# Kernel optimization log

Hardware: AMD Instinct MI355X
Metric: run time of the kernel (lower is better)

The kernel has to match this reference:

```python
import jax, jax.numpy as jnp
import numpy as np

N = 100000
IN_CH = 128
HID = 16
HEADS = 8
OUT_CH = 16
E = 1600000
NEG_SLOPE = 0.2


def glorot(key, shape, fan_in, fan_out):
    lim = jnp.sqrt(6.0 / (fan_in + fan_out)).astype(jnp.float32)
    return jax.random.uniform(key, shape, jnp.float32, -lim, lim)


def setup_inputs() -> dict:
    key = jax.random.key(0)
    ks = jax.random.split(key, 10)
    x = jax.random.normal(ks[0], (N, IN_CH), jnp.float32)
    edge_index = jax.random.randint(ks[1], (2, E), 0, N, jnp.int32)
    # layer 1: GATConv(IN_CH, HID, heads=8), concat=True
    W1 = glorot(ks[2], (IN_CH, HEADS * HID), IN_CH, HEADS * HID)
    att_src1 = glorot(ks[3], (HEADS, HID), HID, 1)
    att_dst1 = glorot(ks[4], (HEADS, HID), HID, 1)
    b1 = jnp.zeros((HEADS * HID,), jnp.float32)
    # layer 2: GATConv(HID*8, OUT_CH, heads=1)
    W2 = glorot(ks[5], (HEADS * HID, OUT_CH), HEADS * HID, OUT_CH)
    att_src2 = glorot(ks[6], (1, OUT_CH), OUT_CH, 1)
    att_dst2 = glorot(ks[7], (1, OUT_CH), OUT_CH, 1)
    b2 = jnp.zeros((OUT_CH,), jnp.float32)
    return {"x": x, "edge_index": edge_index, "W1": W1, "att_src1": att_src1,
            "att_dst1": att_dst1, "b1": b1, "W2": W2, "att_src2": att_src2,
            "att_dst2": att_dst2, "b2": b2}


def gat_layer(x, src, tgt, W, a_src, a_dst, bias, heads, ch, n):
    # h: [N, H, C]
    h = (x @ W).reshape(n, heads, ch)
    alpha_s = jnp.sum(h * a_src[None], axis=-1)  # [N, H]
    alpha_d = jnp.sum(h * a_dst[None], axis=-1)  # [N, H]
    # per-edge attention logit (message flows src -> tgt)
    e = jax.nn.leaky_relu(alpha_s[src] + alpha_d[tgt], NEG_SLOPE)  # [E, H]
    # segment softmax over target node neighborhoods (stable)
    m = jax.ops.segment_max(e, tgt, num_segments=n)  # [N, H]
    e = jnp.exp(e - m[tgt])
    denom = jax.ops.segment_sum(e, tgt, num_segments=n)
    alpha = e / (denom[tgt] + 1e-16)  # [E, H]
    # weighted scatter-add of source features
    out = jax.ops.segment_sum(h[src] * alpha[:, :, None], tgt, num_segments=n)
    return out.reshape(n, heads * ch) + bias


def reference(x, edge_index, W1, att_src1, att_dst1, b1, W2, att_src2, att_dst2, b2):
    n = x.shape[0]
    loops = jnp.arange(n, dtype=edge_index.dtype)
    src = jnp.concatenate([edge_index[0], loops])
    tgt = jnp.concatenate([edge_index[1], loops])
    h = gat_layer(x, src, tgt, W1, att_src1, att_dst1, b1, HEADS, HID, n)
    h = jax.nn.elu(h)
    out = gat_layer(h, src, tgt, W2, att_src2, att_dst2, b2, 1, OUT_CH, n)
    return out
```

## Files before the change

kernel.cpp:

```cpp
#include <hip/hip_runtime.h>
#include <hip/hip_fp16.h>
#include <math.h>

#define IN_CH 128
#define HEADS 8
#define HID 16
#define OUT_CH 16
#define NEG 0.2f
#define NPB 256
#define MAXBUCK 400
#define AST 136

__device__ __forceinline__ float lrelu(float x){ return x > 0.f ? x : NEG * x; }

typedef _Float16 half8 __attribute__((ext_vector_type(8)));
typedef float    f32x4 __attribute__((ext_vector_type(4)));

__global__ __launch_bounds__(256) void k_bhist(const int* __restrict__ tgt, int E, int nbuck, int epb,
                                               int* __restrict__ bcnt){
    __shared__ int hist[MAXBUCK];
    int tid = threadIdx.x;
    for (int i = tid; i < nbuck; i += 256) hist[i] = 0;
    __syncthreads();
    int start = blockIdx.x * epb, end = min(start + epb, E);
    for (int e = start + tid; e < end; e += 256) atomicAdd(&hist[tgt[e] >> 8], 1);
    __syncthreads();
    for (int i = tid; i < nbuck; i += 256) if (hist[i]) atomicAdd(&bcnt[i], hist[i]);
}

__global__ void k_bscan(const int* __restrict__ bcnt, int nbuck, int E,
                        int* __restrict__ boffs, int* __restrict__ bcur){
    __shared__ int s[512];
    int t = threadIdx.x;
    int v = (t < nbuck) ? bcnt[t] : 0;
    int orig = v;
    s[t] = v; __syncthreads();
    for (int off = 1; off < 512; off <<= 1){
        int u = (t >= off) ? s[t - off] : 0;
        __syncthreads();
        v += u; s[t] = v; __syncthreads();
    }
    if (t < nbuck){ boffs[t] = v - orig; bcur[t] = v - orig; }
    if (t == 0) boffs[nbuck] = E;
}

__global__ __launch_bounds__(256) void k_bscatter(const int* __restrict__ ei, int E, int nbuck, int epb,
                                                  int* __restrict__ bcur, int2* __restrict__ ebuck){
    __shared__ int hist[MAXBUCK];
    __shared__ int base[MAXBUCK];
    int tid = threadIdx.x;
    for (int i = tid; i < nbuck; i += 256) hist[i] = 0;
    __syncthreads();
    int start = blockIdx.x * epb, end = min(start + epb, E);
    for (int e = start + tid; e < end; e += 256) atomicAdd(&hist[ei[E + e] >> 8], 1);
    __syncthreads();
    for (int i = tid; i < nbuck; i += 256){
        base[i] = hist[i] ? atomicAdd(&bcur[i], hist[i]) : 0;
        hist[i] = 0;
    }
    __syncthreads();
    for (int e = start + tid; e < end; e += 256){
        int s = ei[e], t = ei[E + e];
        int b = t >> 8;
        int r = atomicAdd(&hist[b], 1);
        ebuck[base[b] + r] = make_int2(s, t);
    }
}

__global__ __launch_bounds__(256) void k_csr(const int2* __restrict__ ebuck, const int* __restrict__ boffs,
                                             int N, int E,
                                             int* __restrict__ offs, int* __restrict__ esrc){
    __shared__ int cnt[256];
    __shared__ int sscan[256];
    __shared__ int wcur[256];
    int b = blockIdx.x;
    int tid = threadIdx.x;
    int n0 = b * 256;
    int nn = min(256, N - n0);
    cnt[tid] = (tid < nn) ? 1 : 0;
    __syncthreads();
    int e0 = boffs[b], e1 = boffs[b + 1];
    for (int e = e0 + tid; e < e1; e += 256) atomicAdd(&cnt[ebuck[e].y & 255], 1);
    __syncthreads();
    int v = cnt[tid], orig = v;
    sscan[tid] = v; __syncthreads();
    for (int off = 1; off < 256; off <<= 1){
        int u = (tid >= off) ? sscan[tid - off] : 0;
        __syncthreads();
        v += u; sscan[tid] = v; __syncthreads();
    }
    int excl = v - orig;
    int gbase = e0 + n0;
    if (tid < nn){
        offs[n0 + tid] = gbase + excl;
        esrc[gbase + excl] = n0 + tid;
    }
    wcur[tid] = excl + 1;
    __syncthreads();
    for (int e = e0 + tid; e < e1; e += 256){
        int2 p = ebuck[e];
        int r = atomicAdd(&wcur[p.y & 255], 1);
        esrc[gbase + r] = p.x;
    }
    if (b == 0 && tid == 0) offs[N] = E + N;
}

__global__ __launch_bounds__(256) void k_gemm1(const float* __restrict__ x, const float* __restrict__ W1,
                                               __half* __restrict__ h1, int N){
    __shared__ _Float16 sA[64*AST];
    __shared__ _Float16 sB[128*AST];
    int tid = threadIdx.x;
    for (int i = tid; i < 128*128; i += 256){
        int k = i >> 7, c = i & 127;
        sB[c*AST + k] = (_Float16)W1[i];
    }
    int row0 = blockIdx.x * 64;
    #pragma unroll
    for (int i = 0; i < 8; ++i){
        int q = i*256 + tid;
        int r = q >> 5, seg = q & 31;
        float4 v = make_float4(0.f,0.f,0.f,0.f);
        if (row0 + r < N) v = *(const float4*)(x + (size_t)(row0+r)*128 + seg*4);
        _Float16* dst = &sA[r*AST + seg*4];
        dst[0]=(_Float16)v.x; dst[1]=(_Float16)v.y; dst[2]=(_Float16)v.z; dst[3]=(_Float16)v.w;
    }
    __syncthreads();
    int wave = tid >> 6, lane = tid & 63;
    int m = lane & 15, quad = lane >> 4;
    int rbase = wave * 16;
    f32x4 acc[8] = {};
    #pragma unroll
    for (int kc = 0; kc < 4; ++kc){
        int kb = kc*32 + quad*8;
        half8 a = *(half8*)(&sA[(rbase + m)*AST + kb]);
        #pragma unroll
        for (int t = 0; t < 8; ++t){
            half8 b = *(half8*)(&sB[(t*16 + m)*AST + kb]);
            acc[t] = __builtin_amdgcn_mfma_f32_16x16x32_f16(a, b, acc[t], 0, 0, 0);
        }
    }
    #pragma unroll
    for (int t = 0; t < 8; ++t){
        #pragma unroll
        for (int j = 0; j < 4; ++j){
            int r = row0 + rbase + quad*4 + j;
            if (r < N) h1[(size_t)r*128 + t*16 + m] = __float2half(acc[t][j]);
        }
    }
}

struct H8 { __half2 v[8]; };

__global__ void k_alpha1(const __half2* __restrict__ h1h, const float* __restrict__ asrc, const float* __restrict__ adst,
                         float* __restrict__ as1, float* __restrict__ ad1, int N){
    int idx = blockIdx.x*blockDim.x + threadIdx.x;
    if (idx >= N*HEADS) return;
    int h = idx & 7;
    int n = idx >> 3;
    H8 blk = *(const H8*)(h1h + (size_t)n*64 + h*8);
    const float2* sp = (const float2*)(asrc + h*16);
    const float2* dp = (const float2*)(adst + h*16);
    float ss = 0.f, dd = 0.f;
    #pragma unroll
    for (int j = 0; j < 8; ++j){
        float2 v = __half22float2(blk.v[j]);
        float2 a = sp[j], b = dp[j];
        ss += v.x*a.x + v.y*a.y;
        dd += v.x*b.x + v.y*b.y;
    }
    as1[idx] = ss; ad1[idx] = dd;
}

__global__ __launch_bounds__(256) void k_agg1(const __half2* __restrict__ h1h, const float* __restrict__ as1,
                                              const float* __restrict__ ad1,
                                              const int* __restrict__ offs, const int* __restrict__ esrc,
                                              const float* __restrict__ b1, __half2* __restrict__ hl2h, int N){
    int wv = threadIdx.x >> 6;
    int l  = threadIdx.x & 63;
    int sub = l >> 5;
    int sl  = l & 31;
    int eo  = sl >> 4;
    int ll  = sl & 15;
    int h   = ll >> 1;
    int n = blockIdx.x*8 + wv*2 + sub;
    bool alive = (n < N);
    float adh = 0.f;
    int e0 = 0, deg = 0;
    if (alive){
        adh = ad1[n*8 + h];
        e0 = offs[n];
        deg = offs[n+1] - e0;
    }
    int degmax = max(deg, __shfl_xor(deg, 32));

    float acc0[8] = {0.f,0.f,0.f,0.f,0.f,0.f,0.f,0.f};
    float acc1[8] = {0.f,0.f,0.f,0.f,0.f,0.f,0.f,0.f};
    float den0 = 0.f, den1 = 0.f;
    for (int i = 0; i < degmax; i += 4){
        int j0 = i + eo, j1 = i + 2 + eo;
        bool v0 = j0 < deg, v1 = j1 < deg;
        int i0 = e0 + (v0 ? j0 : 0);
        int i1 = e0 + (v1 ? j1 : 0);
        int s0 = esrc[i0], s1 = esrc[i1];
        float a0 = as1[s0*8 + h], a1 = as1[s1*8 + h];
        half8 r0 = *(const half8*)(h1h + (size_t)s0*64 + ll*4);
        half8 r1 = *(const half8*)(h1h + (size_t)s1*64 + ll*4);
        float w0 = v0 ? __expf(lrelu(a0 + adh)) : 0.f;
        float w1 = v1 ? __expf(lrelu(a1 + adh)) : 0.f;
        den0 += w0; den1 += w1;
        #pragma unroll
        for (int k = 0; k < 8; ++k){
            acc0[k] += w0 * (float)r0[k];
            acc1[k] += w1 * (float)r1[k];
        }
    }
    float den = den0 + den1;
    float o[8];
    #pragma unroll
    for (int k = 0; k < 8; ++k) o[k] = acc0[k] + acc1[k];
    den += __shfl_xor(den, 16);
    #pragma unroll
    for (int k = 0; k < 8; ++k) o[k] += __shfl_xor(o[k], 16);
    if (!alive || eo) return;
    float rd = 1.f / (den + 1e-16f);
    float4 bb0 = *(const float4*)(b1 + ll*8);
    float4 bb1 = *(const float4*)(b1 + ll*8 + 4);
    float bv[8] = {bb0.x, bb0.y, bb0.z, bb0.w, bb1.x, bb1.y, bb1.z, bb1.w};
    #pragma unroll
    for (int k = 0; k < 8; ++k){
        float t = o[k]*rd + bv[k];
        o[k] = t > 0.f ? t : expm1f(t);
    }
    __half2 q[4];
    #pragma unroll
    for (int k = 0; k < 4; ++k) q[k] = __floats2half2_rn(o[2*k], o[2*k+1]);
    *(float4*)(hl2h + (size_t)n*64 + ll*4) = *(float4*)q;
}

#define FMA4(acc, a, b) { acc.x += (a)*(b).x; acc.y += (a)*(b).y; acc.z += (a)*(b).z; acc.w += (a)*(b).w; }

__global__ __launch_bounds__(256) void k_gemm2(const __half2* __restrict__ hl2h, const float* __restrict__ W2,
                                               const float* __restrict__ asrc2, const float* __restrict__ adst2,
                                               __half2* __restrict__ h2h, float* __restrict__ as2, float* __restrict__ ad2,
                                               int N){
    __shared__ float sX[64*132];
    __shared__ float sW2[128*16];
    int tid = threadIdx.x;
    for (int i = tid; i < 128*16; i += 256) sW2[i] = W2[i];
    int row0 = blockIdx.x * 64;
    #pragma unroll
    for (int i = 0; i < 4; ++i){
        int q = i*256 + tid;
        int r = q >> 4, seg = q & 15;
        float4 raw = make_float4(0.f,0.f,0.f,0.f);
        if (row0 + r < N) raw = ((const float4*)(hl2h + (size_t)(row0+r)*64))[seg];
        const __half2* hp = (const __half2*)&raw;
        float* dst = &sX[r*132 + seg*8];
        #pragma unroll
        for (int j = 0; j < 4; ++j){
            float2 f = __half22float2(hp[j]);
            dst[2*j] = f.x; dst[2*j+1] = f.y;
        }
    }
    __syncthreads();
    int nd = tid >> 2;
    int cq = tid & 3, c0 = cq*4;
    int n = row0 + nd;
    float4 acc = make_float4(0.f,0.f,0.f,0.f);
    #pragma unroll 4
    for (int k4 = 0; k4 < 32; ++k4){
        float4 a  = *(const float4*)(&sX[nd*132 + k4*4]);
        float4 w0 = *(const float4*)(&sW2[(k4*4+0)*16 + c0]);
        float4 w1 = *(const float4*)(&sW2[(k4*4+1)*16 + c0]);
        float4 w2 = *(const float4*)(&sW2[(k4*4+2)*16 + c0]);
        float4 w3 = *(const float4*)(&sW2[(k4*4+3)*16 + c0]);
        FMA4(acc, a.x, w0); FMA4(acc, a.y, w1); FMA4(acc, a.z, w2); FMA4(acc, a.w, w3);
    }
    float ps = acc.x*asrc2[c0] + acc.y*asrc2[c0+1] + acc.z*asrc2[c0+2] + acc.w*asrc2[c0+3];
    float pd = acc.x*adst2[c0] + acc.y*adst2[c0+1] + acc.z*adst2[c0+2] + acc.w*adst2[c0+3];
    ps += __shfl_xor(ps, 1); ps += __shfl_xor(ps, 2);
    pd += __shfl_xor(pd, 1); pd += __shfl_xor(pd, 2);
    if (n < N){
        __half2 p0 = __floats2half2_rn(acc.x, acc.y);
        __half2 p1 = __floats2half2_rn(acc.z, acc.w);
        float2 ov;
        *(__half2*)&ov.x = p0; *(__half2*)&ov.y = p1;
        *(float2*)(h2h + (size_t)n*8 + cq*2) = ov;
        if (cq == 0){ as2[n] = ps; ad2[n] = pd; }
    }
}

__global__ __launch_bounds__(256) void k_agg2(const __half2* __restrict__ h2h, const float* __restrict__ as2v,
                                              const float* __restrict__ ad2v,
                                              const int* __restrict__ offs, const int* __restrict__ esrc,
                                              const float* __restrict__ b2, float* __restrict__ out, int N){
    int n = blockIdx.x*4 + (threadIdx.x >> 6);
    if (n >= N) return;
    int l = threadIdx.x & 63;
    int e0 = offs[n], e1 = offs[n+1];
    float ad = ad2v[n];
    int eo = l >> 3, c2 = l & 7;
    float ax = 0.f, ay = 0.f, den = 0.f;
    for (int e = e0 + eo; e < e1; e += 8){
        int s = esrc[e];
        float w = __expf(lrelu(as2v[s] + ad));
        den += w;
        float2 f = __half22float2(h2h[(size_t)s*8 + c2]);
        ax += w * f.x; ay += w * f.y;
    }
    ax += __shfl_xor(ax, 8);  ay += __shfl_xor(ay, 8);  den += __shfl_xor(den, 8);
    ax += __shfl_xor(ax, 16); ay += __shfl_xor(ay, 16); den += __shfl_xor(den, 16);
    ax += __shfl_xor(ax, 32); ay += __shfl_xor(ay, 32); den += __shfl_xor(den, 32);
    if (eo == 0){
        float rd = 1.f / (den + 1e-16f);
        float2 bb = *(const float2*)(b2 + c2*2);
        float2 o = make_float2(ax*rd + bb.x, ay*rd + bb.y);
        *(float2*)(out + (size_t)n*16 + c2*2) = o;
    }
}

extern "C" void kernel_launch(void* const* d_in, const int* in_sizes, int n_in,
                              void* d_out, int out_size, void* d_ws, size_t ws_size,
                              hipStream_t stream){
    const float* x     = (const float*)d_in[0];
    const int*   ei    = (const int*)  d_in[1];
    const float* W1    = (const float*)d_in[2];
    const float* asrc1 = (const float*)d_in[3];
    const float* adst1 = (const float*)d_in[4];
    const float* b1    = (const float*)d_in[5];
    const float* W2    = (const float*)d_in[6];
    const float* asrc2 = (const float*)d_in[7];
    const float* adst2 = (const float*)d_in[8];
    const float* b2    = (const float*)d_in[9];
    float* out = (float*)d_out;

    const int N = in_sizes[0] / IN_CH;
    const int E = in_sizes[1] / 2;
    const int ETOT = E + N;
    const int NBUCK = (N + NPB - 1) / NPB;

    char* p = (char*)d_ws;
    auto alloc = [&](size_t bytes) -> char* {
        char* r = p; p += (bytes + 255) & ~(size_t)255; return r;
    };
    __half2* h1h  = (__half2*)alloc((size_t)N * 64 * 4);
    __half2* hl2h = (__half2*)alloc((size_t)N * 64 * 4);
    float* as1   = (float*)alloc((size_t)N * 8 * 4);
    float* ad1   = (float*)alloc((size_t)N * 8 * 4);
    __half2* h2h = (__half2*)alloc((size_t)N * 8 * 4);
    float* as2   = (float*)alloc((size_t)N * 4);
    float* ad2   = (float*)alloc((size_t)N * 4);
    int*   bcnt  = (int*)  alloc((size_t)MAXBUCK * 4);
    int*   boffs = (int*)  alloc((size_t)(MAXBUCK + 1) * 4);
    int*   bcur  = (int*)  alloc((size_t)MAXBUCK * 4);
    int*   offs  = (int*)  alloc((size_t)(N + 1) * 4);
    int*   esrc  = (int*)  alloc((size_t)ETOT * 4);
    int2*  ebuck = (int2*)hl2h;

    (void)hipMemsetAsync(bcnt, 0, (size_t)NBUCK * 4, stream);

    const int GPART = 512;
    const int epb = (E + GPART - 1) / GPART;

    k_bhist   <<<GPART, 256, 0, stream>>>(ei + E, E, NBUCK, epb, bcnt);
    k_bscan   <<<1,     512, 0, stream>>>(bcnt, NBUCK, E, boffs, bcur);
    k_bscatter<<<GPART, 256, 0, stream>>>(ei, E, NBUCK, epb, bcur, ebuck);
    k_csr     <<<NBUCK, 256, 0, stream>>>(ebuck, boffs, N, E, offs, esrc);

    k_gemm1  <<<(N + 63) / 64, 256, 0, stream>>>(x, W1, (__half*)h1h, N);
    k_alpha1 <<<(N * HEADS + 255) / 256, 256, 0, stream>>>(h1h, asrc1, adst1, as1, ad1, N);
    k_agg1   <<<(N + 7) / 8, 256, 0, stream>>>(h1h, as1, ad1, offs, esrc, b1, hl2h, N);
    k_gemm2  <<<(N + 63) / 64, 256, 0, stream>>>(hl2h, W2, asrc2, adst2, h2h, as2, ad2, N);
    k_agg2   <<<(N + 3) / 4, 256, 0, stream>>>(h2h, as2, ad2, offs, esrc, b2, out, N);
}
```

Measured before the change: 333.4 us.

## Quantize layer-1 features to per-head int8 for neighbor aggregation gather

The alpha kernel now also quantizes each node's per-head 16-channel fp16 features to offset uint8 with a per-head scale, stored beside the source logit as a float2. The aggregation kernel gathers 16 bytes per head instead of 32, remaps lanes so each lane covers one head across 4 edge slots, and removes the +128 offset with a correction term after the loop. This halves gather traffic in the bandwidth-bound edge aggregation, at the cost of int8 quantization error and more unpack arithmetic. The aggregation launch is also split into two halves over node ranges.

```diff
diff --git a/kernel.cpp b/kernel.cpp
--- a/kernel.cpp
+++ b/kernel.cpp
@@ -152,7 +152,8 @@
 struct H8 { __half2 v[8]; };
 
 __global__ void k_alpha1(const __half2* __restrict__ h1h, const float* __restrict__ asrc, const float* __restrict__ adst,
-                         float* __restrict__ as1, float* __restrict__ ad1, int N){
+                         float2* __restrict__ asw, float* __restrict__ ad1,
+                         unsigned char* __restrict__ h1q, int N){
     int idx = blockIdx.x*blockDim.x + threadIdx.x;
     if (idx >= N*HEADS) return;
     int h = idx & 7;
@@ -160,81 +161,121 @@
     H8 blk = *(const H8*)(h1h + (size_t)n*64 + h*8);
     const float2* sp = (const float2*)(asrc + h*16);
     const float2* dp = (const float2*)(adst + h*16);
+    float fv[16];
     float ss = 0.f, dd = 0.f;
     #pragma unroll
     for (int j = 0; j < 8; ++j){
         float2 v = __half22float2(blk.v[j]);
+        fv[2*j] = v.x; fv[2*j+1] = v.y;
         float2 a = sp[j], b = dp[j];
         ss += v.x*a.x + v.y*a.y;
         dd += v.x*b.x + v.y*b.y;
     }
-    as1[idx] = ss; ad1[idx] = dd;
-}
-
-__global__ __launch_bounds__(256) void k_agg1(const __half2* __restrict__ h1h, const float* __restrict__ as1,
+    float mx = 1e-12f;
+    #pragma unroll
+    for (int k = 0; k < 16; ++k) mx = fmaxf(mx, fabsf(fv[k]));
+    float rs = 127.f / mx;
+    unsigned int w[4];
+    #pragma unroll
+    for (int d = 0; d < 4; ++d){
+        unsigned int b0 = (unsigned int)((int)rintf(fv[4*d+0]*rs) + 128);
+        unsigned int b1 = (unsigned int)((int)rintf(fv[4*d+1]*rs) + 128);
+        unsigned int b2 = (unsigned int)((int)rintf(fv[4*d+2]*rs) + 128);
+        unsigned int b3 = (unsigned int)((int)rintf(fv[4*d+3]*rs) + 128);
+        w[d] = b0 | (b1 << 8) | (b2 << 16) | (b3 << 24);
+    }
+    asw[idx] = make_float2(ss, mx * (1.f/127.f));
+    ad1[idx] = dd;
+    *(uint4*)(h1q + (size_t)idx*16) = make_uint4(w[0], w[1], w[2], w[3]);
+}
+
+__global__ __launch_bounds__(256) void k_agg1(const unsigned char* __restrict__ h1q, const float2* __restrict__ asw,
                                               const float* __restrict__ ad1,
                                               const int* __restrict__ offs, const int* __restrict__ esrc,
-                                              const float* __restrict__ b1, __half2* __restrict__ hl2h, int N){
+                                              const float* __restrict__ b1, __half2* __restrict__ hl2h,
+                                              int nbase, int nend){
     int wv = threadIdx.x >> 6;
     int l  = threadIdx.x & 63;
-    int sub = l >> 5;
-    int sl  = l & 31;
-    int eo  = sl >> 4;
-    int ll  = sl & 15;
-    int h   = ll >> 1;
-    int n = blockIdx.x*8 + wv*2 + sub;
-    bool alive = (n < N);
-    float adh = 0.f;
+    int nsub = l >> 5;
+    int slot = (l >> 3) & 3;
+    int c    = l & 7;
+    int n = nbase + blockIdx.x*8 + wv*2 + nsub;
+    bool alive = (n < nend);
+    float adc = 0.f;
     int e0 = 0, deg = 0;
     if (alive){
-        adh = ad1[n*8 + h];
+        adc = ad1[n*8 + c];
         e0 = offs[n];
         deg = offs[n+1] - e0;
     }
     int degmax = max(deg, __shfl_xor(deg, 32));
 
-    float acc0[8] = {0.f,0.f,0.f,0.f,0.f,0.f,0.f,0.f};
-    float acc1[8] = {0.f,0.f,0.f,0.f,0.f,0.f,0.f,0.f};
+    float acc0[16] = {}; float acc1[16] = {};
     float den0 = 0.f, den1 = 0.f;
-    for (int i = 0; i < degmax; i += 4){
-        int j0 = i + eo, j1 = i + 2 + eo;
+    float dq0 = 0.f,  dq1 = 0.f;
+    for (int i = 0; i < degmax; i += 8){
+        int j0 = i + slot, j1 = i + 4 + slot;
         bool v0 = j0 < deg, v1 = j1 < deg;
-        int i0 = e0 + (v0 ? j0 : 0);
-        int i1 = e0 + (v1 ? j1 : 0);
-        int s0 = esrc[i0], s1 = esrc[i1];
-        float a0 = as1[s0*8 + h], a1 = as1[s1*8 + h];
-        half8 r0 = *(const half8*)(h1h + (size_t)s0*64 + ll*4);
-        half8 r1 = *(const half8*)(h1h + (size_t)s1*64 + ll*4);
-        float w0 = v0 ? __expf(lrelu(a0 + adh)) : 0.f;
-        float w1 = v1 ? __expf(lrelu(a1 + adh)) : 0.f;
+        int iA = e0 + (v0 ? j0 : 0);
+        int iB = e0 + (v1 ? j1 : 0);
+        int s0 = esrc[iA], s1 = esrc[iB];
+        float2 aw0 = asw[s0*8 + c];
+        float2 aw1 = asw[s1*8 + c];
+        uint4 q0 = *(const uint4*)(h1q + (size_t)s0*128 + c*16);
+        uint4 q1 = *(const uint4*)(h1q + (size_t)s1*128 + c*16);
+        float w0 = v0 ? __expf(lrelu(aw0.x + adc)) : 0.f;
+        float w1 = v1 ? __expf(lrelu(aw1.x + adc)) : 0.f;
+        float wq0 = w0 * aw0.y;
+        float wq1 = w1 * aw1.y;
         den0 += w0; den1 += w1;
+        dq0 += wq0; dq1 += wq1;
+        const unsigned int* u0 = (const unsigned int*)&q0;
+        const unsigned int* u1 = (const unsigned int*)&q1;
         #pragma unroll
-        for (int k = 0; k < 8; ++k){
-            acc0[k] += w0 * (float)r0[k];
-            acc1[k] += w1 * (float)r1[k];
+        for (int d = 0; d < 4; ++d){
+            unsigned int a = u0[d], b = u1[d];
+            acc0[4*d+0] += wq0 * (float)(a & 255u);
+            acc0[4*d+1] += wq0 * (float)((a >> 8) & 255u);
+            acc0[4*d+2] += wq0 * (float)((a >> 16) & 255u);
+            acc0[4*d+3] += wq0 * (float)(a >> 24);
+            acc1[4*d+0] += wq1 * (float)(b & 255u);
+            acc1[4*d+1] += wq1 * (float)((b >> 8) & 255u);
+            acc1[4*d+2] += wq1 * (float)((b >> 16) & 255u);
+            acc1[4*d+3] += wq1 * (float)(b >> 24);
         }
     }
     float den = den0 + den1;
-    float o[8];
-    #pragma unroll
-    for (int k = 0; k < 8; ++k) o[k] = acc0[k] + acc1[k];
-    den += __shfl_xor(den, 16);
-    #pragma unroll
-    for (int k = 0; k < 8; ++k) o[k] += __shfl_xor(o[k], 16);
-    if (!alive || eo) return;
+    float dq  = dq0 + dq1;
+    float o[16];
+    #pragma unroll
+    for (int k = 0; k < 16; ++k) o[k] = acc0[k] + acc1[k];
+    den += __shfl_xor(den, 8);  den += __shfl_xor(den, 16);
+    dq  += __shfl_xor(dq, 8);   dq  += __shfl_xor(dq, 16);
+    #pragma unroll
+    for (int k = 0; k < 16; ++k){
+        o[k] += __shfl_xor(o[k], 8);
+        o[k] += __shfl_xor(o[k], 16);
+    }
+    if (!alive || slot) return;
     float rd = 1.f / (den + 1e-16f);
-    float4 bb0 = *(const float4*)(b1 + ll*8);
-    float4 bb1 = *(const float4*)(b1 + ll*8 + 4);
-    float bv[8] = {bb0.x, bb0.y, bb0.z, bb0.w, bb1.x, bb1.y, bb1.z, bb1.w};
-    #pragma unroll
-    for (int k = 0; k < 8; ++k){
-        float t = o[k]*rd + bv[k];
+    float bias128 = 128.f * dq;
+    float bv[16];
+    #pragma unroll
+    for (int g = 0; g < 4; ++g){
+        float4 b4 = *(const float4*)(b1 + c*16 + g*4);
+        bv[4*g+0]=b4.x; bv[4*g+1]=b4.y; bv[4*g+2]=b4.z; bv[4*g+3]=b4.w;
+    }
+    #pragma unroll
+    for (int k = 0; k < 16; ++k){
+        float t = (o[k] - bias128)*rd + bv[k];
         o[k] = t > 0.f ? t : expm1f(t);
     }
-    __half2 q[4];
-    #pragma unroll
-    for (int k = 0; k < 4; ++k) q[k] = __floats2half2_rn(o[2*k], o[2*k+1]);
-    *(float4*)(hl2h + (size_t)n*64 + ll*4) = *(float4*)q;
+    __half2 qh[8];
+    #pragma unroll
+    for (int k = 0; k < 8; ++k) qh[k] = __floats2half2_rn(o[2*k], o[2*k+1]);
+    float4* dst = (float4*)(hl2h + (size_t)n*64 + c*8);
+    dst[0] = ((float4*)qh)[0];
+    dst[1] = ((float4*)qh)[1];
 }
 
 #define FMA4(acc, a, b) { acc.x += (a)*(b).x; acc.y += (a)*(b).y; acc.z += (a)*(b).z; acc.w += (a)*(b).w; }
@@ -345,7 +386,8 @@
     };
     __half2* h1h  = (__half2*)alloc((size_t)N * 64 * 4);
     __half2* hl2h = (__half2*)alloc((size_t)N * 64 * 4);
-    float* as1   = (float*)alloc((size_t)N * 8 * 4);
+    unsigned char* h1q = (unsigned char*)alloc((size_t)N * 128);
+    float2* asw  = (float2*)alloc((size_t)N * 8 * 8);
     float* ad1   = (float*)alloc((size_t)N * 8 * 4);
     __half2* h2h = (__half2*)alloc((size_t)N * 8 * 4);
     float* as2   = (float*)alloc((size_t)N * 4);
@@ -368,8 +410,12 @@
     k_csr     <<<NBUCK, 256, 0, stream>>>(ebuck, boffs, N, E, offs, esrc);
 
     k_gemm1  <<<(N + 63) / 64, 256, 0, stream>>>(x, W1, (__half*)h1h, N);
-    k_alpha1 <<<(N * HEADS + 255) / 256, 256, 0, stream>>>(h1h, asrc1, adst1, as1, ad1, N);
-    k_agg1   <<<(N + 7) / 8, 256, 0, stream>>>(h1h, as1, ad1, offs, esrc, b1, hl2h, N);
+    k_alpha1 <<<(N * HEADS + 255) / 256, 256, 0, stream>>>(h1h, asrc1, adst1, asw, ad1, h1q, N);
+
+    const int NH = ((N / 2) + 7) & ~7;
+    k_agg1 <<<(NH + 7) / 8, 256, 0, stream>>>(h1q, asw, ad1, offs, esrc, b1, hl2h, 0, NH);
+    k_agg1 <<<((N - NH) + 7) / 8, 256, 0, stream>>>(h1q, asw, ad1, offs, esrc, b1, hl2h, NH, N);
+
     k_gemm2  <<<(N + 63) / 64, 256, 0, stream>>>(hl2h, W2, asrc2, adst2, h2h, as2, ad2, N);
     k_agg2   <<<(N + 3) / 4, 256, 0, stream>>>(h2h, as2, ad2, offs, esrc, b2, out, N);
 }
```

Result: no change. 330.3 us (-0.9%).
